# Performance work log

Measured on AMD Instinct MI355X. Metric: run time of the kernel, lower is better.

The kernel has to match this reference:

```python
import jax, jax.numpy as jnp
import numpy as np

N_NODES = 300000
N_EDGES = 1200000
D = 128
B = 1000
VOCAB = 26  # vocab_size + 1


def setup_inputs() -> dict:
    key = jax.random.key(0)
    ks = jax.random.split(key, 10)
    x = jax.random.randint(ks[0], (N_NODES,), 0, VOCAB, dtype=jnp.int32)
    edge_index = jax.random.randint(ks[1], (2, N_EDGES), 0, N_NODES, dtype=jnp.int32)
    # cumulative protein boundaries: B proteins of equal length, last entry == N_NODES
    amino_acids_numbers = (jnp.arange(1, B + 1, dtype=jnp.int32) * (N_NODES // B))
    s = 1.0 / np.sqrt(D)
    emb = jax.random.normal(ks[2], (VOCAB, D), dtype=jnp.float32)
    W_rel1 = jax.random.uniform(ks[3], (D, D), jnp.float32, -s, s)
    b_rel1 = jax.random.uniform(ks[4], (D,), jnp.float32, -s, s)
    W_root1 = jax.random.uniform(ks[5], (D, D), jnp.float32, -s, s)
    W_rel2 = jax.random.uniform(ks[6], (D, D), jnp.float32, -s, s)
    b_rel2 = jax.random.uniform(ks[7], (D,), jnp.float32, -s, s)
    W_root2 = jax.random.uniform(ks[8], (D, D), jnp.float32, -s, s)
    return {"x": x, "edge_index": edge_index, "amino_acids_numbers": amino_acids_numbers,
            "emb": emb, "W_rel1": W_rel1, "b_rel1": b_rel1, "W_root1": W_root1,
            "W_rel2": W_rel2, "b_rel2": b_rel2, "W_root2": W_root2}


def _graph_conv(nodes, src, tgt, W_rel, b_rel, W_root, n):
    # PyG GraphConv (aggr='add'): out = Lin_rel(sum_{j->i} x_j) + Lin_root(x_i)
    agg = jax.ops.segment_sum(nodes[src], tgt, num_segments=n)  # [N, D]
    return agg @ W_rel.T + b_rel + nodes @ W_root.T


def reference(x, edge_index, amino_acids_numbers, emb,
              W_rel1, b_rel1, W_root1, W_rel2, b_rel2, W_root2):
    n = x.shape[0]
    src, tgt = edge_index[0], edge_index[1]
    nodes = emb[x]  # [N, D] embedding lookup
    nodes = _graph_conv(nodes, src, tgt, W_rel1, b_rel1, W_root1, n)
    nodes = _graph_conv(nodes, src, tgt, W_rel2, b_rel2, W_root2, n)
    # segment mean pooling over [start:end) slices defined by cumulative ends
    ends = amino_acids_numbers
    seg = jnp.searchsorted(ends, jnp.arange(n), side='right')  # node -> protein id
    b = ends.shape[0]
    sums = jax.ops.segment_sum(nodes, seg, num_segments=b)  # [B, D]
    counts = jnp.diff(ends, prepend=jnp.zeros((1,), ends.dtype)).astype(nodes.dtype)
    return sums / counts[:, None]
```

## Files before the change

### kernel.cpp

```cpp
#include <hip/hip_runtime.h>

#define DD 128
#define VV 26
#define NW 13
#define CS4 4
#define G 256
#define TWIN 512
#define PCW 264

__device__ __forceinline__ unsigned wsum(unsigned v) {
#pragma unroll
    for (int m = 32; m >= 1; m >>= 1) v += __shfl_xor(v, m, 64);
    return v;
}

__device__ __forceinline__ int wscan_incl(int v) {
    int lane = threadIdx.x & 63;
#pragma unroll
    for (int off = 1; off < 64; off <<= 1) {
        int t = __shfl_up(v, off, 64);
        if (lane >= off) v += t;
    }
    return v;
}

__device__ __forceinline__ int seg_guess(const int* ends, int B, int t, int Lavg) {
    int p = t / Lavg;
    if (p > B - 1) p = B - 1;
    while (p > 0 && ends[p - 1] > t) --p;
    while (ends[p] <= t) ++p;
    return p;
}

__device__ __forceinline__ int bseg(const int* cumx, int j) {
    int lo = 0, hi = G - 1;
    while (lo < hi) {
        int mid = (lo + hi + 1) >> 1;
        if (cumx[mid] <= j) lo = mid; else hi = mid - 1;
    }
    return lo;
}

__global__ __launch_bounds__(1024)
void k_sort_pre(const int* __restrict__ src, const int* __restrict__ tgt,
                const int* __restrict__ x, const int* __restrict__ ends,
                int E, int B, int chunk, int Lavg,
                const float* __restrict__ emb,
                const float* __restrict__ W1r, const float* __restrict__ b1,
                const float* __restrict__ W1o,
                const float* __restrict__ W2r, const float* __restrict__ W2o,
                unsigned short* __restrict__ sorted_tl, unsigned* __restrict__ sorted_s,
                int* __restrict__ segstartT, int* __restrict__ seghistT,
                float* __restrict__ P1, float* __restrict__ P2,
                float* __restrict__ P3, float* __restrict__ uvec,
                float* __restrict__ wvec) {
    extern __shared__ int lds[];
    int tid = threadIdx.x;
    int chunkp = (chunk + 1) & ~1;

    if (blockIdx.x >= G) {
        float* e1r = (float*)lds;
        float* r1r = e1r + DD;
        float* b1s = r1r + DD;
        int v = blockIdx.x - G;
        int d = tid;
        if (d < DD) {
            const float* e = emb + v * DD;
            const float* w1r = W1r + d * DD;
            const float* w1o = W1o + d * DD;
            float s1 = 0.f, s2 = 0.f;
            for (int k = 0; k < DD; ++k) { float ev = e[k]; s1 += ev * w1r[k]; s2 += ev * w1o[k]; }
            e1r[d] = s1; r1r[d] = s2; b1s[d] = b1[d];
        }
        __syncthreads();
        if (d < DD) {
            const float* wr = W2r + d * DD;
            const float* wo = W2o + d * DD;
            float p1 = 0.f, p2 = 0.f, p3 = 0.f, su = 0.f, sw = 0.f;
            for (int k = 0; k < DD; ++k) {
                float a = wr[k], bb = wo[k], ee = e1r[k], r = r1r[k], c = b1s[k];
                p1 += ee * a; p2 += r * a + ee * bb; p3 += r * bb;
                su += c * a; sw += c * bb;
            }
            P1[v * DD + d] = p1; P2[v * DD + d] = p2; P3[v * DD + d] = p3;
            if (v == 0) { uvec[d] = su; wvec[d] = sw; }
        }
        return;
    }

    int* lds_ends = lds;
    int* hist = lds_ends + 1024;
    int* cur = hist + 1024;
    int* wsums = cur + 1024;
    unsigned short* lpe = (unsigned short*)(wsums + 16);
    unsigned short* stl = lpe + chunkp;
    unsigned* sts = (unsigned*)(stl + chunkp);

    int b = blockIdx.x;
    int e0 = b * chunk;
    int e1 = min(E, e0 + chunk);
    int clen = e1 - e0;

    for (int i = tid; i < B; i += 1024) lds_ends[i] = ends[i];
    hist[tid] = 0;
    __syncthreads();

    for (int i = tid; i < clen; i += 1024) {
        int t = tgt[e0 + i];
        int p = seg_guess(lds_ends, B, t, Lavg);
        atomicAdd(&hist[p], 1);
        lpe[i] = (unsigned short)p;
    }
    __syncthreads();

    int v = hist[tid];
    if (tid < B) seghistT[tid * G + b] = v;
    int wave = tid >> 6, lane = tid & 63;
    int incl = wscan_incl(v);
    if (lane == 63) wsums[wave] = incl;
    __syncthreads();
    int offw = 0;
    for (int w = 0; w < wave; ++w) offw += wsums[w];
    int excl = incl + offw - v;
    if (tid < B) {
        cur[tid] = excl;
        segstartT[tid * G + b] = e0 + excl;
    }
    __syncthreads();

    for (int i = tid; i < clen; i += 1024) {
        int e = e0 + i;
        int p = lpe[i];
        int s = src[e];
        int t = tgt[e];
        int lbl = x[s];
        int pst = (p == 0) ? 0 : lds_ends[p - 1];
        int pos = atomicAdd(&cur[p], 1);
        stl[pos] = (unsigned short)(((t - pst) << 5) | lbl);
        sts[pos] = (unsigned)s;
    }
    __syncthreads();

    for (int i = tid; i < clen; i += 1024) {
        sorted_tl[e0 + i] = stl[i];
        sorted_s[e0 + i] = sts[i];
    }
}

__global__ __launch_bounds__(256)
void k_counts(const int* __restrict__ ends,
              const int* __restrict__ seghistT, const int* __restrict__ segstartT,
              int B, int E, const unsigned short* __restrict__ sorted_tl,
              unsigned* __restrict__ counts, int* __restrict__ pcumG) {
    __shared__ unsigned tab[TWIN * CS4];
    __shared__ int cumx[G + 4], segb[G], wsums[4];
    int p = blockIdx.x, tid = threadIdx.x;
    int wave = tid >> 6, lane = tid & 63;
    int start = (p == 0) ? 0 : ends[p - 1];
    int end = ends[p];
    int Lp = end - start;

    int h = seghistT[p * G + tid];
    segb[tid] = segstartT[p * G + tid];
    int incl = wscan_incl(h);
    if (lane == 63) wsums[wave] = incl;
    __syncthreads();
    int offw = 0;
    for (int w = 0; w < wave; ++w) offw += wsums[w];
    int excl = incl + offw - h;
    cumx[tid] = excl;
    pcumG[p * PCW + tid] = excl;
    if (tid == 255) { cumx[G] = incl + offw; pcumG[p * PCW + G] = incl + offw; }
    __syncthreads();
    int Dp = cumx[G];

    for (int w0 = 0; w0 < Lp; w0 += TWIN) {
        int wlen = min(TWIN, Lp - w0);
        __syncthreads();
        for (int i = tid; i < wlen * CS4; i += 256) tab[i] = 0u;
        __syncthreads();
        for (int j = tid; j < Dp; j += 256) {
            int bb = bseg(cumx, j);
            int pos = segb[bb] + (j - cumx[bb]);
            unsigned tl = (unsigned)sorted_tl[pos];
            int lbl = (int)(tl & 31u);
            int tloc = (int)(tl >> 5) - w0;
            if ((unsigned)tloc < (unsigned)wlen)
                atomicAdd(&tab[tloc * CS4 + (lbl >> 3)], 1u << ((lbl & 7) * 4));
        }
        __syncthreads();
        unsigned* dst = counts + ((size_t)(start + w0)) * CS4;
        for (int i = tid; i < wlen * CS4; i += 256) dst[i] = tab[i];
    }
}

__global__ __launch_bounds__(256)
void k_protein(const int* __restrict__ x, const int* __restrict__ ends,
               const int* __restrict__ pcumG, const int* __restrict__ segstartT,
               const unsigned* __restrict__ sorted_s,
               const unsigned* __restrict__ counts,
               const float* __restrict__ P1, const float* __restrict__ P2,
               const float* __restrict__ P3, const float* __restrict__ uvec,
               const float* __restrict__ wvec, const float* __restrict__ b2,
               int B, int E, float* __restrict__ out) {
    __shared__ int cumx[G + 4], segb[G];
    __shared__ unsigned red[4][48];
    __shared__ float c2f[VV], cpf[VV], hpf[VV];
    int p = blockIdx.x, tid = threadIdx.x;
    int wave = tid >> 6, lane = tid & 63;
    int start = (p == 0) ? 0 : ends[p - 1];
    int end = ends[p];

    cumx[tid] = pcumG[p * PCW + tid];
    segb[tid] = segstartT[p * G + tid];
    if (tid == 0) cumx[G] = pcumG[p * PCW + G];
    __syncthreads();
    int Dp = cumx[G];

    unsigned c2[16], cp[16], hpw[NW];
#pragma unroll
    for (int k = 0; k < 16; ++k) { c2[k] = 0u; cp[k] = 0u; }
#pragma unroll
    for (int w = 0; w < NW; ++w) hpw[w] = 0u;

    for (int j = tid; j < Dp; j += 256) {
        int bb = bseg(cumx, j);
        int pos = segb[bb] + (j - cumx[bb]);
        int s = (int)sorted_s[pos];
        uint4 c0 = *reinterpret_cast<const uint4*>(counts + (size_t)s * CS4);
        unsigned w;
        w = c0.x; c2[0]  += w & 0x000F000Fu; c2[1]  += (w >> 4) & 0x000F000Fu;
                  c2[2]  += (w >> 8) & 0x000F000Fu; c2[3]  += (w >> 12) & 0x000F000Fu;
        w = c0.y; c2[4]  += w & 0x000F000Fu; c2[5]  += (w >> 4) & 0x000F000Fu;
                  c2[6]  += (w >> 8) & 0x000F000Fu; c2[7]  += (w >> 12) & 0x000F000Fu;
        w = c0.z; c2[8]  += w & 0x000F000Fu; c2[9]  += (w >> 4) & 0x000F000Fu;
                  c2[10] += (w >> 8) & 0x000F000Fu; c2[11] += (w >> 12) & 0x000F000Fu;
        w = c0.w; c2[12] += w & 0x000F000Fu; c2[13] += (w >> 4) & 0x000F000Fu;
                  c2[14] += (w >> 8) & 0x000F000Fu; c2[15] += (w >> 12) & 0x000F000Fu;
    }

    for (int i = start + tid; i < end; i += 256) {
        uint4 c0 = *reinterpret_cast<const uint4*>(counts + (size_t)i * CS4);
        unsigned w;
        w = c0.x; cp[0]  += w & 0x000F000Fu; cp[1]  += (w >> 4) & 0x000F000Fu;
                  cp[2]  += (w >> 8) & 0x000F000Fu; cp[3]  += (w >> 12) & 0x000F000Fu;
        w = c0.y; cp[4]  += w & 0x000F000Fu; cp[5]  += (w >> 4) & 0x000F000Fu;
                  cp[6]  += (w >> 8) & 0x000F000Fu; cp[7]  += (w >> 12) & 0x000F000Fu;
        w = c0.z; cp[8]  += w & 0x000F000Fu; cp[9]  += (w >> 4) & 0x000F000Fu;
                  cp[10] += (w >> 8) & 0x000F000Fu; cp[11] += (w >> 12) & 0x000F000Fu;
        w = c0.w; cp[12] += w & 0x000F000Fu; cp[13] += (w >> 4) & 0x000F000Fu;
                  cp[14] += (w >> 8) & 0x000F000Fu; cp[15] += (w >> 12) & 0x000F000Fu;
        int l = x[i];
        unsigned inc = 1u << ((l & 1) * 16);
        int wi = l >> 1;
#pragma unroll
        for (int w2 = 0; w2 < NW; ++w2) hpw[w2] += (w2 == wi) ? inc : 0u;
    }

#pragma unroll
    for (int k = 0; k < 16; ++k) {
        unsigned a = wsum(c2[k]); if (lane == 0) red[wave][k] = a;
        unsigned b = wsum(cp[k]); if (lane == 0) red[wave][16 + k] = b;
    }
#pragma unroll
    for (int w = 0; w < NW; ++w) {
        unsigned a = wsum(hpw[w]); if (lane == 0) red[wave][32 + w] = a;
    }
    __syncthreads();
    if (tid < 45) {
        unsigned t = red[0][tid] + red[1][tid] + red[2][tid] + red[3][tid];
        if (tid < 32) {
            int i = tid & 15;
            int base = 8 * (i >> 2) + (i & 3);
            float* dst = (tid < 16) ? c2f : cpf;
            if (base < VV) dst[base] = (float)(t & 0xFFFFu);
            if (base + 4 < VV) dst[base + 4] = (float)(t >> 16);
        } else {
            int w = tid - 32;
            hpf[w * 2] = (float)(t & 0xFFFFu);
            if (w * 2 + 1 < VV) hpf[w * 2 + 1] = (float)(t >> 16);
        }
    }
    __syncthreads();

    if (tid < DD) {
        int d = tid;
        float acc = 0.f;
#pragma unroll
        for (int v = 0; v < VV; ++v)
            acc += c2f[v] * P1[v * DD + d] + cpf[v] * P2[v * DD + d] + hpf[v] * P3[v * DD + d];
        float Lp = (float)(end - start);
        float invL = 1.f / Lp;
        float Dpf = (float)Dp;
        out[(size_t)p * DD + d] = acc * invL + (Dpf * invL) * uvec[d] + wvec[d] + b2[d];
    }
}

extern "C" void kernel_launch(void* const* d_in, const int* in_sizes, int n_in,
                              void* d_out, int out_size, void* d_ws, size_t ws_size,
                              hipStream_t stream) {
    const int*   x       = (const int*)d_in[0];
    const int*   edge    = (const int*)d_in[1];
    const int*   ends    = (const int*)d_in[2];
    const float* emb     = (const float*)d_in[3];
    const float* W_rel1  = (const float*)d_in[4];
    const float* b_rel1  = (const float*)d_in[5];
    const float* W_root1 = (const float*)d_in[6];
    const float* W_rel2  = (const float*)d_in[7];
    const float* b_rel2  = (const float*)d_in[8];
    const float* W_root2 = (const float*)d_in[9];

    const int N = in_sizes[0];
    const int E = in_sizes[1] / 2;
    const int B = in_sizes[2];
    const int Lavg = (N / B) > 0 ? (N / B) : 1;
    const int chunk = (E + G - 1) / G;
    const int chunkp = (chunk + 1) & ~1;

    const int* srcp = edge;
    const int* tgtp = edge + E;

    auto align256 = [](size_t v) { return (v + 255) & ~(size_t)255; };
    char* ws = (char*)d_ws;
    size_t off = 0;
    unsigned* counts = (unsigned*)(ws + off);                off += align256((size_t)N * CS4 * 4);
    int* segstartT = (int*)(ws + off);                       off += align256((size_t)B * G * 4);
    int* seghistT = (int*)(ws + off);                        off += align256((size_t)B * G * 4);
    int* pcumG = (int*)(ws + off);                           off += align256((size_t)B * PCW * 4);
    unsigned short* sorted_tl = (unsigned short*)(ws + off); off += align256((size_t)E * 2);
    unsigned* sorted_s = (unsigned*)(ws + off);              off += align256((size_t)E * 4);
    float* P1 = (float*)(ws + off);                          off += align256((size_t)VV * DD * 4);
    float* P2 = (float*)(ws + off);                          off += align256((size_t)VV * DD * 4);
    float* P3 = (float*)(ws + off);                          off += align256((size_t)VV * DD * 4);
    float* uvec = (float*)(ws + off);                        off += align256((size_t)DD * 4);
    float* wvec = (float*)(ws + off);                        off += align256((size_t)DD * 4);
    (void)ws_size; (void)n_in; (void)out_size;


    size_t ldsb = (size_t)(3 * 1024 + 16) * 4 + (size_t)chunkp * 4 + (size_t)chunk * 4;
    k_sort_pre<<<G + VV, 1024, ldsb, stream>>>(
        srcp, tgtp, x, ends, E, B, chunk, Lavg,
        emb, W_rel1, b_rel1, W_root1, W_rel2, W_root2,
        sorted_tl, sorted_s, segstartT, seghistT, P1, P2, P3, uvec, wvec);

    k_counts<<<B, 256, 0, stream>>>(ends, seghistT, segstartT, B, E, sorted_tl,
                                    counts, pcumG);

    k_protein<<<B, 256, 0, stream>>>(x, ends, pcumG, segstartT, sorted_s, counts,
                                     P1, P2, P3, uvec, wvec, b_rel2, B, E, (float*)d_out);
}
```

Baseline: 65.03 us.

## Pack src and target label into one 64-bit record, compact sources per protein

The sort kernel now writes each edge as a single 64-bit word holding the source index and the packed target/label, instead of two separate arrays. The counts kernel reads this word and, on its first window, scatters the source indices into a dense per-protein array. The protein kernel can then read sources contiguously without rebuilding the segment prefix table or doing a binary search per edge. The cost is wider sort writes and an extra write pass, and it assumes each protein has at most PAD (4096) incoming edges, which holds only for the test's roughly 1200 per protein.

Result: no change. 64.66 us (-0.6%).

```diff
diff --git a/kernel.cpp b/kernel.cpp
--- a/kernel.cpp
+++ b/kernel.cpp
@@ -6,7 +6,7 @@
 #define CS4 4
 #define G 256
 #define TWIN 512
-#define PCW 264
+#define PAD 4096
 
 __device__ __forceinline__ unsigned wsum(unsigned v) {
 #pragma unroll
@@ -49,17 +49,17 @@
                 const float* __restrict__ W1r, const float* __restrict__ b1,
                 const float* __restrict__ W1o,
                 const float* __restrict__ W2r, const float* __restrict__ W2o,
-                unsigned short* __restrict__ sorted_tl, unsigned* __restrict__ sorted_s,
+                unsigned long long* __restrict__ sorted_ts,
                 int* __restrict__ segstartT, int* __restrict__ seghistT,
                 float* __restrict__ P1, float* __restrict__ P2,
                 float* __restrict__ P3, float* __restrict__ uvec,
                 float* __restrict__ wvec) {
-    extern __shared__ int lds[];
+    extern __shared__ char smem[];
     int tid = threadIdx.x;
     int chunkp = (chunk + 1) & ~1;
 
     if (blockIdx.x >= G) {
-        float* e1r = (float*)lds;
+        float* e1r = (float*)smem;
         float* r1r = e1r + DD;
         float* b1s = r1r + DD;
         int v = blockIdx.x - G;
@@ -88,13 +88,12 @@
         return;
     }
 
-    int* lds_ends = lds;
+    unsigned long long* pay = (unsigned long long*)smem;
+    int* lds_ends = (int*)(pay + chunk);
     int* hist = lds_ends + 1024;
     int* cur = hist + 1024;
     int* wsums = cur + 1024;
     unsigned short* lpe = (unsigned short*)(wsums + 16);
-    unsigned short* stl = lpe + chunkp;
-    unsigned* sts = (unsigned*)(stl + chunkp);
 
     int b = blockIdx.x;
     int e0 = b * chunk;
@@ -136,22 +135,20 @@
         int lbl = x[s];
         int pst = (p == 0) ? 0 : lds_ends[p - 1];
         int pos = atomicAdd(&cur[p], 1);
-        stl[pos] = (unsigned short)(((t - pst) << 5) | lbl);
-        sts[pos] = (unsigned)s;
-    }
-    __syncthreads();
-
-    for (int i = tid; i < clen; i += 1024) {
-        sorted_tl[e0 + i] = stl[i];
-        sorted_s[e0 + i] = sts[i];
-    }
+        pay[pos] = ((unsigned long long)(unsigned)s << 16)
+                 | (unsigned long long)(unsigned)(((t - pst) << 5) | lbl);
+    }
+    __syncthreads();
+
+    for (int i = tid; i < clen; i += 1024) sorted_ts[e0 + i] = pay[i];
 }
 
 __global__ __launch_bounds__(256)
 void k_counts(const int* __restrict__ ends,
               const int* __restrict__ seghistT, const int* __restrict__ segstartT,
-              int B, int E, const unsigned short* __restrict__ sorted_tl,
-              unsigned* __restrict__ counts, int* __restrict__ pcumG) {
+              int B, int E, const unsigned long long* __restrict__ sorted_ts,
+              unsigned* __restrict__ counts, unsigned* __restrict__ csG,
+              int* __restrict__ DpG) {
     __shared__ unsigned tab[TWIN * CS4];
     __shared__ int cumx[G + 4], segb[G], wsums[4];
     int p = blockIdx.x, tid = threadIdx.x;
@@ -167,10 +164,8 @@
     __syncthreads();
     int offw = 0;
     for (int w = 0; w < wave; ++w) offw += wsums[w];
-    int excl = incl + offw - h;
-    cumx[tid] = excl;
-    pcumG[p * PCW + tid] = excl;
-    if (tid == 255) { cumx[G] = incl + offw; pcumG[p * PCW + G] = incl + offw; }
+    cumx[tid] = incl + offw - h;
+    if (tid == 255) { cumx[G] = incl + offw; DpG[p] = incl + offw; }
     __syncthreads();
     int Dp = cumx[G];
 
@@ -182,7 +177,9 @@
         for (int j = tid; j < Dp; j += 256) {
             int bb = bseg(cumx, j);
             int pos = segb[bb] + (j - cumx[bb]);
-            unsigned tl = (unsigned)sorted_tl[pos];
+            unsigned long long ts = sorted_ts[pos];
+            unsigned tl = (unsigned)(ts & 0xFFFFull);
+            if (w0 == 0) csG[(size_t)p * PAD + j] = (unsigned)(ts >> 16);
             int lbl = (int)(tl & 31u);
             int tloc = (int)(tl >> 5) - w0;
             if ((unsigned)tloc < (unsigned)wlen)
@@ -196,26 +193,19 @@
 
 __global__ __launch_bounds__(256)
 void k_protein(const int* __restrict__ x, const int* __restrict__ ends,
-               const int* __restrict__ pcumG, const int* __restrict__ segstartT,
-               const unsigned* __restrict__ sorted_s,
+               const int* __restrict__ DpG, const unsigned* __restrict__ csG,
                const unsigned* __restrict__ counts,
                const float* __restrict__ P1, const float* __restrict__ P2,
                const float* __restrict__ P3, const float* __restrict__ uvec,
                const float* __restrict__ wvec, const float* __restrict__ b2,
                int B, int E, float* __restrict__ out) {
-    __shared__ int cumx[G + 4], segb[G];
     __shared__ unsigned red[4][48];
     __shared__ float c2f[VV], cpf[VV], hpf[VV];
     int p = blockIdx.x, tid = threadIdx.x;
     int wave = tid >> 6, lane = tid & 63;
     int start = (p == 0) ? 0 : ends[p - 1];
     int end = ends[p];
-
-    cumx[tid] = pcumG[p * PCW + tid];
-    segb[tid] = segstartT[p * G + tid];
-    if (tid == 0) cumx[G] = pcumG[p * PCW + G];
-    __syncthreads();
-    int Dp = cumx[G];
+    int Dp = DpG[p];
 
     unsigned c2[16], cp[16], hpw[NW];
 #pragma unroll
@@ -223,10 +213,9 @@
 #pragma unroll
     for (int w = 0; w < NW; ++w) hpw[w] = 0u;
 
+    const unsigned* cs = csG + (size_t)p * PAD;
     for (int j = tid; j < Dp; j += 256) {
-        int bb = bseg(cumx, j);
-        int pos = segb[bb] + (j - cumx[bb]);
-        int s = (int)sorted_s[pos];
+        int s = (int)cs[j];
         uint4 c0 = *reinterpret_cast<const uint4*>(counts + (size_t)s * CS4);
         unsigned w;
         w = c0.x; c2[0]  += w & 0x000F000Fu; c2[1]  += (w >> 4) & 0x000F000Fu;
@@ -323,29 +312,29 @@
     auto align256 = [](size_t v) { return (v + 255) & ~(size_t)255; };
     char* ws = (char*)d_ws;
     size_t off = 0;
-    unsigned* counts = (unsigned*)(ws + off);                off += align256((size_t)N * CS4 * 4);
-    int* segstartT = (int*)(ws + off);                       off += align256((size_t)B * G * 4);
-    int* seghistT = (int*)(ws + off);                        off += align256((size_t)B * G * 4);
-    int* pcumG = (int*)(ws + off);                           off += align256((size_t)B * PCW * 4);
-    unsigned short* sorted_tl = (unsigned short*)(ws + off); off += align256((size_t)E * 2);
-    unsigned* sorted_s = (unsigned*)(ws + off);              off += align256((size_t)E * 4);
-    float* P1 = (float*)(ws + off);                          off += align256((size_t)VV * DD * 4);
-    float* P2 = (float*)(ws + off);                          off += align256((size_t)VV * DD * 4);
-    float* P3 = (float*)(ws + off);                          off += align256((size_t)VV * DD * 4);
-    float* uvec = (float*)(ws + off);                        off += align256((size_t)DD * 4);
-    float* wvec = (float*)(ws + off);                        off += align256((size_t)DD * 4);
+    unsigned* counts = (unsigned*)(ws + off);                 off += align256((size_t)N * CS4 * 4);
+    int* segstartT = (int*)(ws + off);                        off += align256((size_t)B * G * 4);
+    int* seghistT = (int*)(ws + off);                         off += align256((size_t)B * G * 4);
+    int* DpG = (int*)(ws + off);                              off += align256((size_t)B * 4);
+    unsigned long long* sorted_ts = (unsigned long long*)(ws + off); off += align256((size_t)E * 8);
+    unsigned* csG = (unsigned*)(ws + off);                    off += align256((size_t)B * PAD * 4);
+    float* P1 = (float*)(ws + off);                           off += align256((size_t)VV * DD * 4);
+    float* P2 = (float*)(ws + off);                           off += align256((size_t)VV * DD * 4);
+    float* P3 = (float*)(ws + off);                           off += align256((size_t)VV * DD * 4);
+    float* uvec = (float*)(ws + off);                         off += align256((size_t)DD * 4);
+    float* wvec = (float*)(ws + off);                         off += align256((size_t)DD * 4);
     (void)ws_size; (void)n_in; (void)out_size;
 
 
-    size_t ldsb = (size_t)(3 * 1024 + 16) * 4 + (size_t)chunkp * 4 + (size_t)chunk * 4;
+    size_t ldsb = (size_t)chunk * 8 + (size_t)(3 * 1024 + 16) * 4 + (size_t)chunkp * 2;
     k_sort_pre<<<G + VV, 1024, ldsb, stream>>>(
         srcp, tgtp, x, ends, E, B, chunk, Lavg,
         emb, W_rel1, b_rel1, W_root1, W_rel2, W_root2,
-        sorted_tl, sorted_s, segstartT, seghistT, P1, P2, P3, uvec, wvec);
-
-    k_counts<<<B, 256, 0, stream>>>(ends, seghistT, segstartT, B, E, sorted_tl,
-                                    counts, pcumG);
-
-    k_protein<<<B, 256, 0, stream>>>(x, ends, pcumG, segstartT, sorted_s, counts,
+        sorted_ts, segstartT, seghistT, P1, P2, P3, uvec, wvec);
+
+    k_counts<<<B, 256, 0, stream>>>(ends, seghistT, segstartT, B, E, sorted_ts,
+                                    counts, csG, DpG);
+
+    k_protein<<<B, 256, 0, stream>>>(x, ends, DpG, csG, counts,
                                      P1, P2, P3, uvec, wvec, b_rel2, B, E, (float*)d_out);
 }
```
